# Optimization experiments

Hardware: AMD Instinct MI355X
Metric: run time of the kernel (lower is better)

The kernel has to match this reference:

```python
import jax, jax.numpy as jnp
import numpy as np

N_NODES = 50000
N_EDGES = 400000
N_GRAPHS = 128
IN_CH = 768
COND = 768
HID = 128
HEADS = 4


def _gat_conv(x, src, dst, W, att_src, att_dst, bias):
    """PyG-style GATConv (concat=True, negative_slope=0.2). x:[N,Fin], W:[Fin,H*D]."""
    N = x.shape[0]
    H, D = att_src.shape
    h = (x @ W).reshape(N, H, D)                      # [N,H,D]
    a_src = jnp.sum(h * att_src, axis=-1)             # [N,H]
    a_dst = jnp.sum(h * att_dst, axis=-1)             # [N,H]
    alpha = jax.nn.leaky_relu(a_src[src] + a_dst[dst], 0.2)   # [E,H]
    m = jax.ops.segment_max(alpha, dst, num_segments=N)       # per-dst max (stable softmax)
    alpha = jnp.exp(alpha - m[dst])
    s = jax.ops.segment_sum(alpha, dst, num_segments=N)
    alpha = alpha / (s[dst] + 1e-16)                  # PyG softmax eps
    msg = h[src] * alpha[:, :, None]                  # [E,H,D]
    out = jax.ops.segment_sum(msg, dst, num_segments=N)       # [N,H,D]
    return out.reshape(N, H * D) + bias


def setup_inputs() -> dict:
    key = jax.random.key(0)
    ks = jax.random.split(key, 12)

    def glorot(k, shape):
        fan = shape[0] + shape[-1]
        return jax.random.normal(k, shape, jnp.float32) * jnp.sqrt(2.0 / fan)

    x = jax.random.normal(ks[0], (N_NODES, IN_CH), jnp.float32)
    substring_embed = jax.random.normal(ks[1], (N_GRAPHS, COND), jnp.float32)
    edge_index = jax.random.randint(ks[2], (2, N_EDGES), 0, N_NODES)
    batch = jnp.sort(jax.random.randint(ks[3], (N_NODES,), 0, N_GRAPHS))

    W1 = glorot(ks[4], (IN_CH + COND, HEADS * HID))
    att_src1 = glorot(ks[5], (HEADS, HID))
    att_dst1 = glorot(ks[6], (HEADS, HID))
    b1 = jnp.zeros((HEADS * HID,), jnp.float32)

    W2 = glorot(ks[7], (HEADS * HID, 1 * HID))
    att_src2 = glorot(ks[8], (1, HID))
    att_dst2 = glorot(ks[9], (1, HID))
    b2 = jnp.zeros((HID,), jnp.float32)

    out_W = glorot(ks[10], (HID, 1))
    out_b = jnp.zeros((1,), jnp.float32)

    return {"x": x, "substring_embed": substring_embed,
            "W1": W1, "att_src1": att_src1, "att_dst1": att_dst1, "b1": b1,
            "W2": W2, "att_src2": att_src2, "att_dst2": att_dst2, "b2": b2,
            "out_W": out_W, "out_b": out_b,
            "edge_index": edge_index, "batch": batch}


def reference(x, substring_embed, W1, att_src1, att_dst1, b1,
              W2, att_src2, att_dst2, b2, out_W, out_b,
              edge_index, batch):
    N = x.shape[0]
    loops = jnp.arange(N)                              # PyG add_self_loops=True
    src = jnp.concatenate([edge_index[0], loops])
    dst = jnp.concatenate([edge_index[1], loops])

    h = jnp.concatenate([x, substring_embed[batch]], axis=-1)   # [N, IN+COND]
    h = jax.nn.relu(_gat_conv(h, src, dst, W1, att_src1, att_dst1, b1))
    h = jax.nn.relu(_gat_conv(h, src, dst, W2, att_src2, att_dst2, b2))
    out = (h @ out_W + out_b)[:, 0]                    # squeeze(-1) -> [N]
    return out
```

## Files before the change

### kernel.cpp

```cpp
#include <hip/hip_runtime.h>
#include <hip/hip_bf16.h>
#include <cstdint>
#include <cstddef>

#define NN 50000
#define NE 400000
#define NG 128
#define INCH 768
#define CONDCH 768
#define HIDD 128
#define NHEAD 4
#define F1 (NHEAD * HIDD)
#define F2 HIDD
#define MPAD 50176
#define CAP 64

typedef unsigned short ushort_t;
typedef float f32x4 __attribute__((ext_vector_type(4)));
typedef __bf16 bf16x8 __attribute__((ext_vector_type(8)));

typedef const void __attribute__((address_space(1))) as1_void;
typedef void __attribute__((address_space(3))) as3_void;

__device__ __forceinline__ void gload_lds16(const void* g, void* l) {
    __builtin_amdgcn_global_load_lds((as1_void*)g, (as3_void*)l, 16, 0, 0);
}

__device__ __forceinline__ ushort_t f2bf(float f) {
    uint32_t u = __float_as_uint(f);
    uint32_t r = (u + 0x7fffu + ((u >> 16) & 1u)) >> 16;
    return (ushort_t)r;
}
__device__ __forceinline__ uint32_t pack2(float a, float b) {
    return (uint32_t)f2bf(a) | ((uint32_t)f2bf(b) << 16);
}
__device__ __forceinline__ float bf_lo(uint32_t u) { return __uint_as_float(u << 16); }
__device__ __forceinline__ float bf_hi(uint32_t u) { return __uint_as_float(u & 0xffff0000u); }

#define R1 (F1 * INCH)
#define R2 (R1 + F1 * CONDCH)
#define R3 (R2 + F2 * F1)
#define CND4 (NG * CONDCH / 4)
__global__ __launch_bounds__(256) void k_prep(
    const float* __restrict__ W1, const float* __restrict__ W2, const float* __restrict__ cond,
    ushort_t* __restrict__ W1aT, ushort_t* __restrict__ W1cT, ushort_t* __restrict__ W2T,
    ushort_t* __restrict__ condb, int* __restrict__ cursor, int* __restrict__ csr_src)
{
    int idx = blockIdx.x * blockDim.x + threadIdx.x;
    if (idx < NN) {
        cursor[idx] = 1;
        csr_src[(size_t)idx * CAP] = idx;
    }
    if (idx < CND4) {
        float4 v = *(const float4*)(cond + (size_t)idx * 4);
        ushort4 o;
        o.x = f2bf(v.x); o.y = f2bf(v.y); o.z = f2bf(v.z); o.w = f2bf(v.w);
        *(ushort4*)(condb + (size_t)idx * 4) = o;
    }
    if (idx >= R3) return;
    if (idx < R1) {
        int n = idx / INCH, k = idx % INCH;
        W1aT[idx] = f2bf(W1[(size_t)k * F1 + n]);
    } else if (idx < R2) {
        int j = idx - R1;
        int n = j / CONDCH, k = j % CONDCH;
        W1cT[j] = f2bf(W1[(size_t)(INCH + k) * F1 + n]);
    } else {
        int j = idx - R2;
        int n = j / F1, k = j % F1;
        W2T[j] = f2bf(W2[(size_t)k * F2 + n]);
    }
}

__global__ __launch_bounds__(256) void k_scat(const int* __restrict__ ei,
                                              int* __restrict__ cursor,
                                              int* __restrict__ csr_src) {
    int e = blockIdx.x * blockDim.x + threadIdx.x;
    if (e >= NE) return;
    int src = ei[e];
    int dst = ei[NE + e];
    int pos = atomicAdd(&cursor[dst], 1);
    csr_src[(size_t)dst * CAP + pos] = src;
}

template <int TM, bool A_F32, bool ADD_GATHER, bool OUT_BF16, bool FUSE_ATT>
__global__ __launch_bounds__(TM * 2, 4) void k_mgemm(
    const ushort_t* __restrict__ A, const float* __restrict__ Af, int Arowmax,
    const ushort_t* __restrict__ BT, void* __restrict__ Cv,
    int M, int N, int K, int nBN,
    const float* __restrict__ G, const int* __restrict__ gidx,
    const float* __restrict__ attS, const float* __restrict__ attD,
    float* __restrict__ aS, float* __restrict__ aD, int attStride)
{
    constexpr int SAB = A_F32 ? TM * 128 : TM * 64;
    constexpr int SB = 8192;
    constexpr int ISS_BYTES = TM * 32;
    __shared__ __align__(16) char smem[2 * SAB + 2 * SB];
    char* sA = smem;
    char* sB = smem + 2 * SAB;

    const int nwg = gridDim.x;
    const int orig = blockIdx.x;
    const int q = nwg >> 3, r = nwg & 7;
    const int xcd = orig & 7, sid = orig >> 3;
    const int wg = (xcd < r ? xcd * (q + 1) : r * (q + 1) + (xcd - r) * q) + sid;
    const int bx = wg / nBN, by = wg % nBN;

    const int tid = threadIdx.x;
    const int lane = tid & 63;
    const int wave = tid >> 6;
    const int wr = wave >> 1, wc = wave & 1;
    const int m0 = bx * TM, n0 = by * 128;

    const int sr = tid >> 2;
    const int sc = (tid & 3) * 8;
    const ushort_t* gA = A_F32 ? nullptr : (A + (size_t)(m0 + sr) * K + sc);
    const ushort_t* gB = BT + (size_t)(n0 + sr) * K + sc;
    const int ldsw = wave * 1024;

    const float* gAf_base[4];
    if constexpr (A_F32) {
        const int rowInIss = tid >> 3;
        const int chunkS = (tid & 7) ^ (rowInIss & 7);
#pragma unroll
        for (int j = 0; j < 4; j++) {
            int rr = m0 + j * (TM / 4) + rowInIss;
            if (rr > Arowmax) rr = Arowmax;
            gAf_base[j] = Af + (size_t)rr * K + chunkS * 4;
        }
    }

    const int a_off = (wr * 64 + (lane & 15)) * 64 + (lane >> 4) * 16;
    const int b_off = (wc * 64 + (lane & 15)) * 64 + (lane >> 4) * 16;

    auto STAGE = [&](int kt, int b) {
        if constexpr (A_F32) {
#pragma unroll
            for (int j = 0; j < 4; j++)
                gload_lds16(gAf_base[j] + kt, sA + b * SAB + j * ISS_BYTES + ldsw);
        } else {
            char* dA = sA + b * SAB + ldsw;
            gload_lds16(gA + kt, dA);
            gload_lds16(gA + (size_t)(TM / 2) * K + kt, dA + SAB / 2);
        }
        char* dB = sB + b * SB + ldsw;
        gload_lds16(gB + kt, dB);
        if (TM == 128)
            gload_lds16(gB + (size_t)64 * K + kt, dB + 4096);
    };

    f32x4 acc[4][4];
#pragma unroll
    for (int i = 0; i < 4; i++)
#pragma unroll
        for (int j = 0; j < 4; j++) acc[i][j] = 0.f;

    STAGE(0, 0);
    const int nt = K / 32;
    for (int t = 0; t < nt; t++) {
        const int cur = t & 1;
        asm volatile("s_waitcnt vmcnt(0)" ::: "memory");
        __builtin_amdgcn_s_barrier();
        __builtin_amdgcn_sched_barrier(0);
        if (t + 1 < nt) STAGE((t + 1) * 32, cur ^ 1);
        bf16x8 af[4], bfr[4];
        if constexpr (A_F32) {
            const int q32 = (lane >> 4) * 32;
#pragma unroll
            for (int i = 0; i < 4; i++) {
                int rw = wr * 64 + i * 16 + (lane & 15);
                int sw = (rw & 7) << 4;
                const char* base = sA + cur * SAB + rw * 128;
                float4 lo = *(const float4*)(base + (q32 ^ sw));
                float4 hi = *(const float4*)(base + ((q32 + 16) ^ sw));
                bf16x8 v;
                v[0] = (__bf16)lo.x; v[1] = (__bf16)lo.y; v[2] = (__bf16)lo.z; v[3] = (__bf16)lo.w;
                v[4] = (__bf16)hi.x; v[5] = (__bf16)hi.y; v[6] = (__bf16)hi.z; v[7] = (__bf16)hi.w;
                af[i] = v;
            }
        } else {
#pragma unroll
            for (int i = 0; i < 4; i++) af[i] = *(const bf16x8*)(sA + cur * SAB + a_off + i * 1024);
        }
#pragma unroll
        for (int j = 0; j < 4; j++) bfr[j] = *(const bf16x8*)(sB + cur * SB + b_off + j * 1024);
#pragma unroll
        for (int i = 0; i < 4; i++)
#pragma unroll
            for (int j = 0; j < 4; j++)
                acc[i][j] = __builtin_amdgcn_mfma_f32_16x16x32_bf16(af[i], bfr[j], acc[i][j], 0, 0, 0);
    }

    float asv[4], adv[4];
    if (FUSE_ATT) {
#pragma unroll
        for (int j = 0; j < 4; j++) {
            int col = wc * 64 + j * 16 + (lane & 15);
            asv[j] = attS[by * 128 + col];
            adv[j] = attD[by * 128 + col];
        }
    }
    float* redS = (float*)smem;
    float* redD = (float*)smem + 2 * TM;

#pragma unroll
    for (int i = 0; i < 4; i++) {
        int mbase = m0 + wr * 64 + i * 16 + (lane >> 4) * 4;
#pragma unroll
        for (int rr = 0; rr < 4; rr++) {
            int m = mbase + rr;
            if (m >= M) continue;
            const float* grow = nullptr;
            if (ADD_GATHER) grow = G + (size_t)gidx[m] * N;
            float vs = 0.f, vd = 0.f;
#pragma unroll
            for (int j = 0; j < 4; j++) {
                int n = n0 + wc * 64 + j * 16 + (lane & 15);
                float v = acc[i][j][rr];
                if (ADD_GATHER) v += grow[n];
                if (OUT_BF16) ((ushort_t*)Cv)[(size_t)m * N + n] = f2bf(v);
                else          ((float*)Cv)[(size_t)m * N + n] = v;
                if (FUSE_ATT) { vs = fmaf(v, asv[j], vs); vd = fmaf(v, adv[j], vd); }
            }
            if (FUSE_ATT) {
#pragma unroll
                for (int o = 1; o < 16; o <<= 1) { vs += __shfl_xor(vs, o); vd += __shfl_xor(vd, o); }
                if ((lane & 15) == 0) {
                    int mloc = wr * 64 + i * 16 + (lane >> 4) * 4 + rr;
                    redS[wc * TM + mloc] = vs;
                    redD[wc * TM + mloc] = vd;
                }
            }
        }
    }
    if (FUSE_ATT) {
        __syncthreads();
        int sd = tid >= TM ? 1 : 0, mloc = tid & (TM - 1);
        int m = m0 + mloc;
        if (m < M) {
            const float* rb = sd ? redD : redS;
            float v = rb[mloc] + rb[TM + mloc];
            (sd ? aD : aS)[(size_t)m * attStride + by] = v;
        }
    }
}

__global__ __launch_bounds__(256) void k_agg1(
    const ushort_t* __restrict__ h1, const float* __restrict__ a_src, const float* __restrict__ a_dst,
    const int* __restrict__ cnt, const int* __restrict__ csr_src,
    const float* __restrict__ b1, ushort_t* __restrict__ g1)
{
    const int n = blockIdx.x * 4 + (threadIdx.x >> 6);
    const int lane = threadIdx.x & 63;
    const int head = lane >> 4;
    const int beg = n * CAP;
    const int end = beg + cnt[n];
    const float4 ad = *(const float4*)(a_dst + (size_t)n * 4);

    float mx[4] = {-1e30f, -1e30f, -1e30f, -1e30f};
    for (int p = beg + lane; p < end; p += 64) {
        int src = csr_src[p];
        float4 as = *(const float4*)(a_src + (size_t)src * 4);
        float v;
        v = as.x + ad.x; v = v >= 0.f ? v : 0.2f * v; mx[0] = fmaxf(mx[0], v);
        v = as.y + ad.y; v = v >= 0.f ? v : 0.2f * v; mx[1] = fmaxf(mx[1], v);
        v = as.z + ad.z; v = v >= 0.f ? v : 0.2f * v; mx[2] = fmaxf(mx[2], v);
        v = as.w + ad.w; v = v >= 0.f ? v : 0.2f * v; mx[3] = fmaxf(mx[3], v);
    }
#pragma unroll
    for (int o = 32; o; o >>= 1) {
        mx[0] = fmaxf(mx[0], __shfl_xor(mx[0], o));
        mx[1] = fmaxf(mx[1], __shfl_xor(mx[1], o));
        mx[2] = fmaxf(mx[2], __shfl_xor(mx[2], o));
        mx[3] = fmaxf(mx[3], __shfl_xor(mx[3], o));
    }
    const float m   = (head & 1) ? ((head & 2) ? mx[3] : mx[1]) : ((head & 2) ? mx[2] : mx[0]);
    const float adh = (head & 1) ? ((head & 2) ? ad.w : ad.y)   : ((head & 2) ? ad.z : ad.x);

    float ssum = 0.f;
    float a[8] = {0.f, 0.f, 0.f, 0.f, 0.f, 0.f, 0.f, 0.f};
    int p = beg;
#define LREL(l) ((l) >= 0.f ? (l) : 0.2f * (l))
#define ACC8(c, u) \
        a[0] = fmaf(c, bf_lo(u.x), a[0]); a[1] = fmaf(c, bf_hi(u.x), a[1]); \
        a[2] = fmaf(c, bf_lo(u.y), a[2]); a[3] = fmaf(c, bf_hi(u.y), a[3]); \
        a[4] = fmaf(c, bf_lo(u.z), a[4]); a[5] = fmaf(c, bf_hi(u.z), a[5]); \
        a[6] = fmaf(c, bf_lo(u.w), a[6]); a[7] = fmaf(c, bf_hi(u.w), a[7]);
    for (; p + 3 < end; p += 4) {
        int4 s4 = *(const int4*)(csr_src + p);
        uint4 u0 = *(const uint4*)(h1 + (size_t)s4.x * F1 + lane * 8);
        uint4 u1 = *(const uint4*)(h1 + (size_t)s4.y * F1 + lane * 8);
        uint4 u2 = *(const uint4*)(h1 + (size_t)s4.z * F1 + lane * 8);
        uint4 u3 = *(const uint4*)(h1 + (size_t)s4.w * F1 + lane * 8);
        float c0 = expf(LREL(a_src[s4.x * 4 + head] + adh) - m);
        float c1 = expf(LREL(a_src[s4.y * 4 + head] + adh) - m);
        float c2 = expf(LREL(a_src[s4.z * 4 + head] + adh) - m);
        float c3 = expf(LREL(a_src[s4.w * 4 + head] + adh) - m);
        ssum += c0 + c1 + c2 + c3;
        ACC8(c0, u0) ACC8(c1, u1) ACC8(c2, u2) ACC8(c3, u3)
    }
    for (; p < end; p++) {
        int s0 = csr_src[p];
        uint4 u0 = *(const uint4*)(h1 + (size_t)s0 * F1 + lane * 8);
        float c0 = expf(LREL(a_src[s0 * 4 + head] + adh) - m);
        ssum += c0;
        ACC8(c0, u0)
    }
#undef ACC8
    const float inv = 1.0f / (ssum + 1e-16f);
    const int ch = lane * 8;
    float4 bA = *(const float4*)(b1 + ch);
    float4 bB = *(const float4*)(b1 + ch + 4);
    uint4 ov;
    ov.x = pack2(fmaxf(fmaf(a[0], inv, bA.x), 0.f), fmaxf(fmaf(a[1], inv, bA.y), 0.f));
    ov.y = pack2(fmaxf(fmaf(a[2], inv, bA.z), 0.f), fmaxf(fmaf(a[3], inv, bA.w), 0.f));
    ov.z = pack2(fmaxf(fmaf(a[4], inv, bB.x), 0.f), fmaxf(fmaf(a[5], inv, bB.y), 0.f));
    ov.w = pack2(fmaxf(fmaf(a[6], inv, bB.z), 0.f), fmaxf(fmaf(a[7], inv, bB.w), 0.f));
    *(uint4*)(g1 + (size_t)n * F1 + ch) = ov;
}

__global__ __launch_bounds__(256) void k_agg2(
    const ushort_t* __restrict__ h2, const float* __restrict__ a_src, const float* __restrict__ a_dst,
    const int* __restrict__ cnt, const int* __restrict__ csr_src,
    const float* __restrict__ b2, const float* __restrict__ outW, const float* __restrict__ outb,
    float* __restrict__ out)
{
    const int n = blockIdx.x * 4 + (threadIdx.x >> 6);
    const int lane = threadIdx.x & 63;
    const int beg = n * CAP;
    const int end = beg + cnt[n];
    const float ad = a_dst[n];

    float mx = -1e30f;
    for (int p = beg + lane; p < end; p += 64) {
        float v = a_src[csr_src[p]] + ad;
        v = v >= 0.f ? v : 0.2f * v;
        mx = fmaxf(mx, v);
    }
#pragma unroll
    for (int o = 32; o; o >>= 1) mx = fmaxf(mx, __shfl_xor(mx, o));

    float ssum = 0.f;
    float a0 = 0.f, a1 = 0.f;
    int p = beg;
    for (; p + 3 < end; p += 4) {
        int4 s4 = *(const int4*)(csr_src + p);
        uint32_t u0 = *(const uint32_t*)(h2 + (size_t)s4.x * F2 + lane * 2);
        uint32_t u1 = *(const uint32_t*)(h2 + (size_t)s4.y * F2 + lane * 2);
        uint32_t u2 = *(const uint32_t*)(h2 + (size_t)s4.z * F2 + lane * 2);
        uint32_t u3 = *(const uint32_t*)(h2 + (size_t)s4.w * F2 + lane * 2);
        float c0 = expf(LREL(a_src[s4.x] + ad) - mx);
        float c1 = expf(LREL(a_src[s4.y] + ad) - mx);
        float c2 = expf(LREL(a_src[s4.z] + ad) - mx);
        float c3 = expf(LREL(a_src[s4.w] + ad) - mx);
        ssum += c0 + c1 + c2 + c3;
        a0 = fmaf(c0, bf_lo(u0), a0); a1 = fmaf(c0, bf_hi(u0), a1);
        a0 = fmaf(c1, bf_lo(u1), a0); a1 = fmaf(c1, bf_hi(u1), a1);
        a0 = fmaf(c2, bf_lo(u2), a0); a1 = fmaf(c2, bf_hi(u2), a1);
        a0 = fmaf(c3, bf_lo(u3), a0); a1 = fmaf(c3, bf_hi(u3), a1);
    }
    for (; p < end; p++) {
        int s0 = csr_src[p];
        uint32_t u0 = *(const uint32_t*)(h2 + (size_t)s0 * F2 + lane * 2);
        float c0 = expf(LREL(a_src[s0] + ad) - mx);
        ssum += c0;
        a0 = fmaf(c0, bf_lo(u0), a0); a1 = fmaf(c0, bf_hi(u0), a1);
    }
    const float inv = 1.0f / (ssum + 1e-16f);
    float v0 = fmaf(a0, inv, b2[lane * 2]);     v0 = v0 > 0.f ? v0 : 0.f;
    float v1 = fmaf(a1, inv, b2[lane * 2 + 1]); v1 = v1 > 0.f ? v1 : 0.f;
    float pr = v0 * outW[lane * 2] + v1 * outW[lane * 2 + 1];
    for (int o = 32; o; o >>= 1) pr += __shfl_xor(pr, o);
    if (lane == 0) out[n] = pr + outb[0];
}

extern "C" void kernel_launch(void* const* d_in, const int* in_sizes, int n_in,
                              void* d_out, int out_size, void* d_ws, size_t ws_size,
                              hipStream_t stream)
{
    const float* x        = (const float*)d_in[0];
    const float* cond     = (const float*)d_in[1];
    const float* W1       = (const float*)d_in[2];
    const float* att_src1 = (const float*)d_in[3];
    const float* att_dst1 = (const float*)d_in[4];
    const float* b1       = (const float*)d_in[5];
    const float* W2       = (const float*)d_in[6];
    const float* att_src2 = (const float*)d_in[7];
    const float* att_dst2 = (const float*)d_in[8];
    const float* b2       = (const float*)d_in[9];
    const float* outW     = (const float*)d_in[10];
    const float* outb     = (const float*)d_in[11];
    const int*   ei       = (const int*)d_in[12];
    const int*   batch    = (const int*)d_in[13];
    float* out = (float*)d_out;

    char* ws = (char*)d_ws;
    size_t off = 0;
    auto alloc = [&](size_t bytes) { void* p = ws + off; off += (bytes + 255) & ~size_t(255); return p; };
    ushort_t* condb   = (ushort_t*)alloc((size_t)NG * CONDCH * 2);
    ushort_t* W1aT    = (ushort_t*)alloc((size_t)F1 * INCH * 2);
    ushort_t* W1cT    = (ushort_t*)alloc((size_t)F1 * CONDCH * 2);
    ushort_t* W2T     = (ushort_t*)alloc((size_t)F2 * F1 * 2);
    float*    C2      = (float*)alloc((size_t)NG * F1 * 4);
    ushort_t* h1b     = (ushort_t*)alloc((size_t)NN * F1 * 2);
    float*    a_src1  = (float*)alloc((size_t)NN * NHEAD * 4);
    float*    a_dst1  = (float*)alloc((size_t)NN * NHEAD * 4);
    int*      cursor  = (int*)alloc((size_t)NN * 4);
    int*      csr_src = (int*)alloc((size_t)NN * CAP * 4);
    ushort_t* g1b     = (ushort_t*)alloc((size_t)MPAD * F1 * 2);
    ushort_t* h2b     = (ushort_t*)alloc((size_t)NN * F2 * 2);
    float*    a_src2  = (float*)alloc((size_t)NN * 4);
    float*    a_dst2  = (float*)alloc((size_t)NN * 4);
    (void)ws_size;

    k_prep<<<(R3 + 255) / 256, 256, 0, stream>>>(W1, W2, cond, W1aT, W1cT, W2T, condb,
                                                 cursor, csr_src);

    k_scat<<<(NE + 255) / 256, 256, 0, stream>>>(ei, cursor, csr_src);

    k_mgemm<128, false, false, false, false><<<4, 256, 0, stream>>>(
        condb, nullptr, 0, W1cT, C2, NG, F1, CONDCH, 4,
        nullptr, nullptr, nullptr, nullptr, nullptr, nullptr, 0);
    k_mgemm<128, true, true, true, true><<<(MPAD / 128) * 4, 256, 0, stream>>>(
        nullptr, x, NN - 1, W1aT, h1b, NN, F1, INCH, 4,
        C2, batch, att_src1, att_dst1, a_src1, a_dst1, NHEAD);
    k_agg1<<<NN / 4, 256, 0, stream>>>(h1b, a_src1, a_dst1, cursor, csr_src, b1, g1b);
    k_mgemm<128, false, false, true, true><<<MPAD / 128, 256, 0, stream>>>(
        g1b, nullptr, 0, W2T, h2b, NN, F2, F1, 1,
        nullptr, nullptr, att_src2, att_dst2, a_src2, a_dst2, 1);
    k_agg2<<<NN / 4, 256, 0, stream>>>(h2b, a_src2, a_dst2, cursor, csr_src, b2, outW, outb, out);
}
```

Baseline: 293.0 us.

## Use dedicated wide-N GEMM for layer-1 so fp32 x is read once

```diff
diff --git a/kernel.cpp b/kernel.cpp
--- a/kernel.cpp
+++ b/kernel.cpp
@@ -83,21 +83,141 @@
     csr_src[(size_t)dst * CAP + pos] = src;
 }
 
-template <int TM, bool A_F32, bool ADD_GATHER, bool OUT_BF16, bool FUSE_ATT>
-__global__ __launch_bounds__(TM * 2, 4) void k_mgemm(
-    const ushort_t* __restrict__ A, const float* __restrict__ Af, int Arowmax,
-    const ushort_t* __restrict__ BT, void* __restrict__ Cv,
-    int M, int N, int K, int nBN,
-    const float* __restrict__ G, const int* __restrict__ gidx,
+__global__ __launch_bounds__(512, 4) void k_gemm1w(
+    const float* __restrict__ Af, const ushort_t* __restrict__ BT,
+    ushort_t* __restrict__ Cv, const float* __restrict__ C2, const int* __restrict__ gidx,
     const float* __restrict__ attS, const float* __restrict__ attD,
-    float* __restrict__ aS, float* __restrict__ aD, int attStride)
+    float* __restrict__ aS, float* __restrict__ aD)
 {
-    constexpr int SAB = A_F32 ? TM * 128 : TM * 64;
-    constexpr int SB = 8192;
-    constexpr int ISS_BYTES = TM * 32;
-    __shared__ __align__(16) char smem[2 * SAB + 2 * SB];
+    constexpr int SAB = 64 * 128;
+    constexpr int SBB = 512 * 64;
+    __shared__ __align__(16) char smem[2 * SAB + 2 * SBB];
     char* sA = smem;
     char* sB = smem + 2 * SAB;
+
+    const int tid = threadIdx.x;
+    const int lane = tid & 63;
+    const int wave = tid >> 6;
+    const int m0 = blockIdx.x * 64;
+
+    const int arow = tid >> 3;
+    const int achunk = (tid & 7) ^ (arow & 7);
+    int ar = m0 + arow; if (ar > NN - 1) ar = NN - 1;
+    const float* gAf = Af + (size_t)ar * INCH + achunk * 4;
+
+    const int bro = tid >> 2;
+    const int bco = (tid & 3) * 8;
+    const ushort_t* gB0 = BT + (size_t)bro * INCH + bco;
+    const int ldsw = wave * 1024;
+
+    const int b_off = (wave * 64 + (lane & 15)) * 64 + (lane >> 4) * 16;
+    const int q32 = (lane >> 4) * 32;
+
+    auto STAGE = [&](int kt, int b) {
+        gload_lds16(gAf + kt, sA + b * SAB + ldsw);
+#pragma unroll
+        for (int j = 0; j < 4; j++)
+            gload_lds16(gB0 + (size_t)j * 128 * INCH + kt, sB + b * SBB + j * 8192 + ldsw);
+    };
+
+    f32x4 acc[4][4];
+#pragma unroll
+    for (int i = 0; i < 4; i++)
+#pragma unroll
+        for (int j = 0; j < 4; j++) acc[i][j] = 0.f;
+
+    STAGE(0, 0);
+    const int nt = INCH / 32;
+    for (int t = 0; t < nt; t++) {
+        const int cur = t & 1;
+        asm volatile("s_waitcnt vmcnt(0)" ::: "memory");
+        __builtin_amdgcn_s_barrier();
+        __builtin_amdgcn_sched_barrier(0);
+        if (t + 1 < nt) STAGE((t + 1) * 32, cur ^ 1);
+        bf16x8 af[4], bfr[4];
+#pragma unroll
+        for (int i = 0; i < 4; i++) {
+            int rw = i * 16 + (lane & 15);
+            int sw = (rw & 7) << 4;
+            const char* base = sA + cur * SAB + rw * 128;
+            float4 lo = *(const float4*)(base + (q32 ^ sw));
+            float4 hi = *(const float4*)(base + ((q32 + 16) ^ sw));
+            bf16x8 v;
+            v[0] = (__bf16)lo.x; v[1] = (__bf16)lo.y; v[2] = (__bf16)lo.z; v[3] = (__bf16)lo.w;
+            v[4] = (__bf16)hi.x; v[5] = (__bf16)hi.y; v[6] = (__bf16)hi.z; v[7] = (__bf16)hi.w;
+            af[i] = v;
+        }
+#pragma unroll
+        for (int j = 0; j < 4; j++) bfr[j] = *(const bf16x8*)(sB + cur * SBB + b_off + j * 1024);
+#pragma unroll
+        for (int i = 0; i < 4; i++)
+#pragma unroll
+            for (int j = 0; j < 4; j++)
+                acc[i][j] = __builtin_amdgcn_mfma_f32_16x16x32_bf16(af[i], bfr[j], acc[i][j], 0, 0, 0);
+    }
+
+    float asv[4], adv[4];
+#pragma unroll
+    for (int j = 0; j < 4; j++) {
+        int n = wave * 64 + j * 16 + (lane & 15);
+        asv[j] = attS[n];
+        adv[j] = attD[n];
+    }
+    float* redS = (float*)smem;
+    float* redD = (float*)smem + 512;
+
+#pragma unroll
+    for (int i = 0; i < 4; i++) {
+#pragma unroll
+        for (int rr = 0; rr < 4; rr++) {
+            int mloc = i * 16 + (lane >> 4) * 4 + rr;
+            int m = m0 + mloc;
+            if (m >= NN) continue;
+            const float* grow = C2 + (size_t)gidx[m] * F1;
+            float vs = 0.f, vd = 0.f;
+#pragma unroll
+            for (int j = 0; j < 4; j++) {
+                int n = wave * 64 + j * 16 + (lane & 15);
+                float v = acc[i][j][rr] + grow[n];
+                Cv[(size_t)m * F1 + n] = f2bf(v);
+                vs = fmaf(v, asv[j], vs);
+                vd = fmaf(v, adv[j], vd);
+            }
+#pragma unroll
+            for (int o = 1; o < 16; o <<= 1) { vs += __shfl_xor(vs, o); vd += __shfl_xor(vd, o); }
+            if ((lane & 15) == 0) {
+                redS[wave * 64 + mloc] = vs;
+                redD[wave * 64 + mloc] = vd;
+            }
+        }
+    }
+    __syncthreads();
+    {
+        int sd = tid >> 8;
+        int rem = tid & 255;
+        int h = rem >> 6;
+        int mloc = rem & 63;
+        int m = m0 + mloc;
+        if (m < NN) {
+            const float* rb = sd ? redD : redS;
+            float v = rb[(2 * h) * 64 + mloc] + rb[(2 * h + 1) * 64 + mloc];
+            (sd ? aD : aS)[(size_t)m * NHEAD + h] = v;
+        }
+    }
+}
+
+template <int TM, bool OUT_BF16, bool FUSE_ATT>
+__global__ __launch_bounds__(TM * 2) void k_mgemm(
+    const ushort_t* __restrict__ A, const ushort_t* __restrict__ BT, void* __restrict__ Cv,
+    int M, int N, int K, int nBN,
+    const float* __restrict__ attS, const float* __restrict__ attD,
+    float* __restrict__ aS, float* __restrict__ aD)
+{
+    constexpr int SA = TM * 64;
+    constexpr int SB = 8192;
+    __shared__ __align__(16) char smem[2 * SA + 2 * SB];
+    char* sA = smem;
+    char* sB = smem + 2 * SA;
 
     const int nwg = gridDim.x;
     const int orig = blockIdx.x;
@@ -114,35 +234,17 @@
 
     const int sr = tid >> 2;
     const int sc = (tid & 3) * 8;
-    const ushort_t* gA = A_F32 ? nullptr : (A + (size_t)(m0 + sr) * K + sc);
+    const ushort_t* gA = A + (size_t)(m0 + sr) * K + sc;
     const ushort_t* gB = BT + (size_t)(n0 + sr) * K + sc;
     const int ldsw = wave * 1024;
 
-    const float* gAf_base[4];
-    if constexpr (A_F32) {
-        const int rowInIss = tid >> 3;
-        const int chunkS = (tid & 7) ^ (rowInIss & 7);
-#pragma unroll
-        for (int j = 0; j < 4; j++) {
-            int rr = m0 + j * (TM / 4) + rowInIss;
-            if (rr > Arowmax) rr = Arowmax;
-            gAf_base[j] = Af + (size_t)rr * K + chunkS * 4;
-        }
-    }
-
     const int a_off = (wr * 64 + (lane & 15)) * 64 + (lane >> 4) * 16;
     const int b_off = (wc * 64 + (lane & 15)) * 64 + (lane >> 4) * 16;
 
     auto STAGE = [&](int kt, int b) {
-        if constexpr (A_F32) {
-#pragma unroll
-            for (int j = 0; j < 4; j++)
-                gload_lds16(gAf_base[j] + kt, sA + b * SAB + j * ISS_BYTES + ldsw);
-        } else {
-            char* dA = sA + b * SAB + ldsw;
-            gload_lds16(gA + kt, dA);
-            gload_lds16(gA + (size_t)(TM / 2) * K + kt, dA + SAB / 2);
-        }
+        char* dA = sA + b * SA + ldsw;
+        gload_lds16(gA + kt, dA);
+        gload_lds16(gA + (size_t)(TM / 2) * K + kt, dA + SA / 2);
         char* dB = sB + b * SB + ldsw;
         gload_lds16(gB + kt, dB);
         if (TM == 128)
@@ -164,24 +266,8 @@
         __builtin_amdgcn_sched_barrier(0);
         if (t + 1 < nt) STAGE((t + 1) * 32, cur ^ 1);
         bf16x8 af[4], bfr[4];
-        if constexpr (A_F32) {
-            const int q32 = (lane >> 4) * 32;
-#pragma unroll
-            for (int i = 0; i < 4; i++) {
-                int rw = wr * 64 + i * 16 + (lane & 15);
-                int sw = (rw & 7) << 4;
-                const char* base = sA + cur * SAB + rw * 128;
-                float4 lo = *(const float4*)(base + (q32 ^ sw));
-                float4 hi = *(const float4*)(base + ((q32 + 16) ^ sw));
-                bf16x8 v;
-                v[0] = (__bf16)lo.x; v[1] = (__bf16)lo.y; v[2] = (__bf16)lo.z; v[3] = (__bf16)lo.w;
-                v[4] = (__bf16)hi.x; v[5] = (__bf16)hi.y; v[6] = (__bf16)hi.z; v[7] = (__bf16)hi.w;
-                af[i] = v;
-            }
-        } else {
-#pragma unroll
-            for (int i = 0; i < 4; i++) af[i] = *(const bf16x8*)(sA + cur * SAB + a_off + i * 1024);
-        }
+#pragma unroll
+        for (int i = 0; i < 4; i++) af[i]  = *(const bf16x8*)(sA + cur * SA + a_off + i * 1024);
 #pragma unroll
         for (int j = 0; j < 4; j++) bfr[j] = *(const bf16x8*)(sB + cur * SB + b_off + j * 1024);
 #pragma unroll
@@ -210,14 +296,11 @@
         for (int rr = 0; rr < 4; rr++) {
             int m = mbase + rr;
             if (m >= M) continue;
-            const float* grow = nullptr;
-            if (ADD_GATHER) grow = G + (size_t)gidx[m] * N;
             float vs = 0.f, vd = 0.f;
 #pragma unroll
             for (int j = 0; j < 4; j++) {
                 int n = n0 + wc * 64 + j * 16 + (lane & 15);
                 float v = acc[i][j][rr];
-                if (ADD_GATHER) v += grow[n];
                 if (OUT_BF16) ((ushort_t*)Cv)[(size_t)m * N + n] = f2bf(v);
                 else          ((float*)Cv)[(size_t)m * N + n] = v;
                 if (FUSE_ATT) { vs = fmaf(v, asv[j], vs); vd = fmaf(v, adv[j], vd); }
@@ -240,7 +323,7 @@
         if (m < M) {
             const float* rb = sd ? redD : redS;
             float v = rb[mloc] + rb[TM + mloc];
-            (sd ? aD : aS)[(size_t)m * attStride + by] = v;
+            (sd ? aD : aS)[m] = v;
         }
     }
 }
@@ -418,15 +501,16 @@
 
     k_scat<<<(NE + 255) / 256, 256, 0, stream>>>(ei, cursor, csr_src);
 
-    k_mgemm<128, false, false, false, false><<<4, 256, 0, stream>>>(
-        condb, nullptr, 0, W1cT, C2, NG, F1, CONDCH, 4,
-        nullptr, nullptr, nullptr, nullptr, nullptr, nullptr, 0);
-    k_mgemm<128, true, true, true, true><<<(MPAD / 128) * 4, 256, 0, stream>>>(
-        nullptr, x, NN - 1, W1aT, h1b, NN, F1, INCH, 4,
-        C2, batch, att_src1, att_dst1, a_src1, a_dst1, NHEAD);
+    k_mgemm<128, false, false><<<4, 256, 0, stream>>>(
+        condb, W1cT, C2, NG, F1, CONDCH, 4, nullptr, nullptr, nullptr, nullptr);
+
+    k_gemm1w<<<MPAD / 64, 512, 0, stream>>>(
+        x, W1aT, h1b, C2, batch, att_src1, att_dst1, a_src1, a_dst1);
+
     k_agg1<<<NN / 4, 256, 0, stream>>>(h1b, a_src1, a_dst1, cursor, csr_src, b1, g1b);
-    k_mgemm<128, false, false, true, true><<<MPAD / 128, 256, 0, stream>>>(
-        g1b, nullptr, 0, W2T, h2b, NN, F2, F1, 1,
-        nullptr, nullptr, att_src2, att_dst2, a_src2, a_dst2, 1);
+
+    k_mgemm<128, true, true><<<MPAD / 128, 256, 0, stream>>>(
+        g1b, W2T, h2b, NN, F2, F1, 1, att_src2, att_dst2, a_src2, a_dst2);
+
     k_agg2<<<NN / 4, 256, 0, stream>>>(h2b, a_src2, a_dst2, cursor, csr_src, b2, outW, outb, out);
 }
```

Result: faster. 284.1 us (-3.0%).
